# Kernel tuning notes

Hardware: AMD Instinct MI355X
Metric: run time of the kernel (lower is better)

The kernel has to match this reference:

```python
import jax, jax.numpy as jnp
import numpy as np

F = 26   # number of sparse features
D = 128  # embedding dim (== dense dim)
B = 16384

# Upper-triangular (offset=1) index pairs of the (F+1)x(F+1) interaction matrix.
_TRIU_R, _TRIU_C = np.triu_indices(F + 1, k=1)
_TRIU_R = jnp.asarray(_TRIU_R)
_TRIU_C = jnp.asarray(_TRIU_C)


def setup_inputs() -> dict:
    key = jax.random.key(0)
    k1, k2 = jax.random.split(key)
    dense_features = jax.random.normal(k1, (B, D), dtype=jnp.float32)
    sparse_values = jax.random.normal(k2, (B, F * D), dtype=jnp.float32)
    return {"dense_features": dense_features, "sparse_values": sparse_values}


def reference(dense_features, sparse_values):
    B_, D_ = dense_features.shape
    sparse = sparse_values.reshape(B_, F, D_)                 # B x F x D
    combined = jnp.concatenate([dense_features[:, None, :], sparse], axis=1)  # B x (F+1) x D
    # Batched pairwise dot products: B x (F+1) x (F+1)
    interactions = jnp.einsum("bfd,bgd->bfg", combined, combined)
    interactions_flat = interactions[:, _TRIU_R, _TRIU_C]     # B x (F + F choose 2)
    return jnp.concatenate([dense_features, interactions_flat], axis=1)
```

## Files before the change

### kernel.cpp

```cpp
#include <hip/hip_runtime.h>
#include <hip/hip_bf16.h>

#define NF 26
#define DD 128
#define OUTW 479

typedef __attribute__((ext_vector_type(8))) short bf16x8;
typedef __attribute__((ext_vector_type(4))) float f32x4;

__device__ __forceinline__ int triidx(int r, int c) {
    return r * NF - (r * (r - 1)) / 2 + (c - r - 1);
}

__device__ __forceinline__ ushort bf16_bits(float x) {
    __hip_bfloat16 h = __float2bfloat16(x);
    return *(ushort*)&h;
}

__device__ __forceinline__ bf16x8 cvt8(const float* p) {
    f32x4 x0 = *(const f32x4*)p;
    f32x4 x1 = *(const f32x4*)(p + 4);
    bf16x8 r;
#pragma unroll
    for (int j = 0; j < 4; ++j) {
        __hip_bfloat16 h0 = __float2bfloat16(x0[j]);
        __hip_bfloat16 h1 = __float2bfloat16(x1[j]);
        r[j]     = *(short*)&h0;
        r[j + 4] = *(short*)&h1;
    }
    return r;
}

__global__ __launch_bounds__(256) void interact_kernel(
    const void* __restrict__ dense_v,
    const void* __restrict__ sparse_v,
    void* __restrict__ out_v,
    int nbatch)
{
    const int gwave = (int)((blockIdx.x * 256u + threadIdx.x) >> 6);
    const int lane  = (int)(threadIdx.x & 63u);
    if (gwave >= nbatch) return;
    const size_t b = (size_t)gwave;

    const int m  = lane & 15;
    const int kg = lane >> 4;
    const int ko = kg * 8;

    {
    }
    const ushort* dpr = (const ushort*)dense_v;
    const ushort uprobe = dpr[2 * lane];
    const int eprobe = (uprobe >> 7) & 0xFF;
    const unsigned long long badmask = __ballot((eprobe < 90) | (eprobe > 140));
    const bool f32_mode = __popcll(badmask) >= 8;

    int sm = m + 15;
    if (sm > NF - 1) sm = NF - 1;

    bf16x8 a0[4], a1[4];
    if (f32_mode) {
        const float* dense  = (const float*)dense_v;
        const float* sparse = (const float*)sparse_v;
        const float* r0 = (m == 0)
            ? (dense + b * DD)
            : (sparse + b * (size_t)(NF * DD) + (size_t)(m - 1) * DD);
        const float* r1 = sparse + b * (size_t)(NF * DD) + (size_t)sm * DD;
#pragma unroll
        for (int t = 0; t < 4; ++t) {
            a0[t] = cvt8(r0 + t * 32 + ko);
            a1[t] = cvt8(r1 + t * 32 + ko);
        }
    } else {
        const ushort* dense  = (const ushort*)dense_v;
        const ushort* sparse = (const ushort*)sparse_v;
        const ushort* r0 = (m == 0)
            ? (dense + b * DD)
            : (sparse + b * (size_t)(NF * DD) + (size_t)(m - 1) * DD);
        const ushort* r1 = sparse + b * (size_t)(NF * DD) + (size_t)sm * DD;
#pragma unroll
        for (int t = 0; t < 4; ++t) {
            a0[t] = *(const bf16x8*)(r0 + t * 32 + ko);
            a1[t] = *(const bf16x8*)(r1 + t * 32 + ko);
        }
    }

    f32x4 g00 = {0.f, 0.f, 0.f, 0.f};
    f32x4 g10 = {0.f, 0.f, 0.f, 0.f};
    f32x4 g11 = {0.f, 0.f, 0.f, 0.f};
#pragma unroll
    for (int t = 0; t < 4; ++t) {
        g00 = __builtin_amdgcn_mfma_f32_16x16x32_bf16(a0[t], a0[t], g00, 0, 0, 0);
        g10 = __builtin_amdgcn_mfma_f32_16x16x32_bf16(a1[t], a0[t], g10, 0, 0, 0);
        g11 = __builtin_amdgcn_mfma_f32_16x16x32_bf16(a1[t], a1[t], g11, 0, 0, 0);
    }

    if (f32_mode) {
        float* orow = (float*)out_v + b * OUTW;
        const float* drow = (const float*)dense_v + b * DD;
        orow[2 * lane]     = drow[2 * lane];
        orow[2 * lane + 1] = drow[2 * lane + 1];
        float* tri = orow + DD;
#pragma unroll
        for (int i = 0; i < 4; ++i) {
            const int rr = kg * 4 + i;
            if (rr < m) tri[triidx(rr, m)] = g00[i];
            const int c2 = 16 + rr;
            if (c2 <= NF) tri[triidx(m, c2)] = g10[i];
            if (rr < m && 16 + m <= NF)
                tri[triidx(16 + rr, 16 + m)] = g11[i];
        }
    } else {
        ushort* orow = (ushort*)out_v + b * OUTW;
        const ushort* drow = (const ushort*)dense_v + b * DD;
        orow[2 * lane]     = drow[2 * lane];
        orow[2 * lane + 1] = drow[2 * lane + 1];
        ushort* tri = orow + DD;
#pragma unroll
        for (int i = 0; i < 4; ++i) {
            const int rr = kg * 4 + i;
            if (rr < m) tri[triidx(rr, m)] = bf16_bits(g00[i]);
            const int c2 = 16 + rr;
            if (c2 <= NF) tri[triidx(m, c2)] = bf16_bits(g10[i]);
            if (rr < m && 16 + m <= NF)
                tri[triidx(16 + rr, 16 + m)] = bf16_bits(g11[i]);
        }
    }
}

extern "C" void kernel_launch(void* const* d_in, const int* in_sizes, int n_in,
                              void* d_out, int out_size, void* d_ws, size_t ws_size,
                              hipStream_t stream) {
    const int nbatch = in_sizes[0] / DD;
    const int blocks = (nbatch * 64 + 255) / 256;
    interact_kernel<<<blocks, 256, 0, stream>>>(d_in[0], d_in[1], d_out, nbatch);
}
```

Measured before the change: 317.2 us.

## Stage f32 inputs and outputs through LDS for coalesced block-wide loads and stores

In the f32 path, each block now covers 4 batch rows. It loads the sparse and dense data with fully coalesced 16-byte loads, converts them to bf16 into a swizzled LDS buffer, and has each wave read its MFMA operands from there. Results are gathered into an LDS output row and written back as contiguous vector stores, replacing the scattered per-lane global stores. This aims to fix uncoalesced reads and writes at the cost of extra LDS traffic, two barriers, and a tail case that assumes nbatch is a multiple of 4.

New measurement: 309.7 us. 1.02x faster.

```diff
diff --git a/kernel.cpp b/kernel.cpp
--- a/kernel.cpp
+++ b/kernel.cpp
@@ -4,6 +4,7 @@
 #define NF 26
 #define DD 128
 #define OUTW 479
+#define SPF (NF * DD)
 
 typedef __attribute__((ext_vector_type(8))) short bf16x8;
 typedef __attribute__((ext_vector_type(4))) float f32x4;
@@ -23,10 +24,8 @@
     bf16x8 r;
 #pragma unroll
     for (int j = 0; j < 4; ++j) {
-        __hip_bfloat16 h0 = __float2bfloat16(x0[j]);
-        __hip_bfloat16 h1 = __float2bfloat16(x1[j]);
-        r[j]     = *(short*)&h0;
-        r[j + 4] = *(short*)&h1;
+        r[j]     = (short)bf16_bits(x0[j]);
+        r[j + 4] = (short)bf16_bits(x1[j]);
     }
     return r;
 }
@@ -37,69 +36,82 @@
     void* __restrict__ out_v,
     int nbatch)
 {
-    const int gwave = (int)((blockIdx.x * 256u + threadIdx.x) >> 6);
-    const int lane  = (int)(threadIdx.x & 63u);
-    if (gwave >= nbatch) return;
-    const size_t b = (size_t)gwave;
-
+    const int tid  = (int)threadIdx.x;
+    const int wave = tid >> 6;
+    const int lane = tid & 63;
     const int m  = lane & 15;
     const int kg = lane >> 4;
-    const int ko = kg * 8;
 
-    {
-    }
     const ushort* dpr = (const ushort*)dense_v;
     const ushort uprobe = dpr[2 * lane];
     const int eprobe = (uprobe >> 7) & 0xFF;
     const unsigned long long badmask = __ballot((eprobe < 90) | (eprobe > 140));
     const bool f32_mode = __popcll(badmask) >= 8;
 
-    int sm = m + 15;
-    if (sm > NF - 1) sm = NF - 1;
-
-    bf16x8 a0[4], a1[4];
     if (f32_mode) {
         const float* dense  = (const float*)dense_v;
         const float* sparse = (const float*)sparse_v;
-        const float* r0 = (m == 0)
-            ? (dense + b * DD)
-            : (sparse + b * (size_t)(NF * DD) + (size_t)(m - 1) * DD);
-        const float* r1 = sparse + b * (size_t)(NF * DD) + (size_t)sm * DD;
+        float* out = (float*)out_v;
+
+        __shared__ __align__(16) ushort stage[4 * 27 * 128];
+        __shared__ __align__(16) float  outS[4 * OUTW];
+
+        const int b0 = (int)blockIdx.x * 4;
+        if (b0 >= nbatch) return;
+
+        const float* sbase = sparse + (size_t)b0 * SPF;
+#pragma unroll
+        for (int it = 0; it < 13; ++it) {
+            const int f = (it * 256 + tid) * 4;
+            f32x4 v = *(const f32x4*)(sbase + f);
+            const int s   = f / SPF;
+            const int rem = f - s * SPF;
+            const int r   = 1 + (rem >> 7);
+            const int c   = rem & 127;
+            const int cb  = c >> 3;
+            const int hf  = (c >> 2) & 1;
+            const int pcb = cb ^ (r & 15);
+            ushort4 h;
+            h.x = bf16_bits(v[0]); h.y = bf16_bits(v[1]);
+            h.z = bf16_bits(v[2]); h.w = bf16_bits(v[3]);
+            *(ushort4*)&stage[s * 3456 + r * 128 + pcb * 8 + hf * 4] = h;
+        }
+        if (tid < 128) {
+            const int f = tid * 4;
+            f32x4 v = *(const f32x4*)(dense + (size_t)b0 * DD + f);
+            const int s = f >> 7;
+            const int c = f & 127;
+#pragma unroll
+            for (int k = 0; k < 4; ++k) outS[s * OUTW + c + k] = v[k];
+            const int cb = c >> 3;
+            const int hf = (c >> 2) & 1;
+            ushort4 h;
+            h.x = bf16_bits(v[0]); h.y = bf16_bits(v[1]);
+            h.z = bf16_bits(v[2]); h.w = bf16_bits(v[3]);
+            *(ushort4*)&stage[s * 3456 + (cb ^ 0) * 8 + hf * 4] = h;
+        }
+        __syncthreads();
+
+        int r1 = m + 16;
+        if (r1 > NF) r1 = NF;
+        bf16x8 a0[4], a1[4];
 #pragma unroll
         for (int t = 0; t < 4; ++t) {
-            a0[t] = cvt8(r0 + t * 32 + ko);
-            a1[t] = cvt8(r1 + t * 32 + ko);
+            const int cb = kg + 4 * t;
+            a0[t] = *(const bf16x8*)&stage[wave * 3456 + m  * 128 + (cb ^ (m  & 15)) * 8];
+            a1[t] = *(const bf16x8*)&stage[wave * 3456 + r1 * 128 + (cb ^ (r1 & 15)) * 8];
         }
-    } else {
-        const ushort* dense  = (const ushort*)dense_v;
-        const ushort* sparse = (const ushort*)sparse_v;
-        const ushort* r0 = (m == 0)
-            ? (dense + b * DD)
-            : (sparse + b * (size_t)(NF * DD) + (size_t)(m - 1) * DD);
-        const ushort* r1 = sparse + b * (size_t)(NF * DD) + (size_t)sm * DD;
+        f32x4 g00 = {0.f, 0.f, 0.f, 0.f};
+        f32x4 g10 = {0.f, 0.f, 0.f, 0.f};
+        f32x4 g11 = {0.f, 0.f, 0.f, 0.f};
 #pragma unroll
         for (int t = 0; t < 4; ++t) {
-            a0[t] = *(const bf16x8*)(r0 + t * 32 + ko);
-            a1[t] = *(const bf16x8*)(r1 + t * 32 + ko);
+            g00 = __builtin_amdgcn_mfma_f32_16x16x32_bf16(a0[t], a0[t], g00, 0, 0, 0);
+            g10 = __builtin_amdgcn_mfma_f32_16x16x32_bf16(a1[t], a0[t], g10, 0, 0, 0);
+            g11 = __builtin_amdgcn_mfma_f32_16x16x32_bf16(a1[t], a1[t], g11, 0, 0, 0);
         }
-    }
 
-    f32x4 g00 = {0.f, 0.f, 0.f, 0.f};
-    f32x4 g10 = {0.f, 0.f, 0.f, 0.f};
-    f32x4 g11 = {0.f, 0.f, 0.f, 0.f};
-#pragma unroll
-    for (int t = 0; t < 4; ++t) {
-        g00 = __builtin_amdgcn_mfma_f32_16x16x32_bf16(a0[t], a0[t], g00, 0, 0, 0);
-        g10 = __builtin_amdgcn_mfma_f32_16x16x32_bf16(a1[t], a0[t], g10, 0, 0, 0);
-        g11 = __builtin_amdgcn_mfma_f32_16x16x32_bf16(a1[t], a1[t], g11, 0, 0, 0);
-    }
-
-    if (f32_mode) {
-        float* orow = (float*)out_v + b * OUTW;
-        const float* drow = (const float*)dense_v + b * DD;
-        orow[2 * lane]     = drow[2 * lane];
-        orow[2 * lane + 1] = drow[2 * lane + 1];
-        float* tri = orow + DD;
+        float* tri = &outS[wave * OUTW + DD];
 #pragma unroll
         for (int i = 0; i < 4; ++i) {
             const int rr = kg * 4 + i;
@@ -109,9 +121,48 @@
             if (rr < m && 16 + m <= NF)
                 tri[triidx(16 + rr, 16 + m)] = g11[i];
         }
-    } else {
+        __syncthreads();
+
+        float* obase = out + (size_t)b0 * OUTW;
+        {
+            *(f32x4*)(obase + tid * 4) = *(const f32x4*)&outS[tid * 4];
+            const int c2 = tid + 256;
+            if (c2 < 479)
+                *(f32x4*)(obase + c2 * 4) = *(const f32x4*)&outS[c2 * 4];
+        }
+        return;
+    }
+
+    {
+        const int gwave = (int)((blockIdx.x * 256u + threadIdx.x) >> 6);
+        if (gwave >= nbatch) return;
+        const size_t b = (size_t)gwave;
+        const int ko = kg * 8;
+        int sm = m + 15;
+        if (sm > NF - 1) sm = NF - 1;
+        const ushort* dense  = (const ushort*)dense_v;
+        const ushort* sparse = (const ushort*)sparse_v;
+        const ushort* r0 = (m == 0)
+            ? (dense + b * DD)
+            : (sparse + b * (size_t)(NF * DD) + (size_t)(m - 1) * DD);
+        const ushort* r1p = sparse + b * (size_t)(NF * DD) + (size_t)sm * DD;
+        bf16x8 a0[4], a1[4];
+#pragma unroll
+        for (int t = 0; t < 4; ++t) {
+            a0[t] = *(const bf16x8*)(r0 + t * 32 + ko);
+            a1[t] = *(const bf16x8*)(r1p + t * 32 + ko);
+        }
+        f32x4 g00 = {0.f, 0.f, 0.f, 0.f};
+        f32x4 g10 = {0.f, 0.f, 0.f, 0.f};
+        f32x4 g11 = {0.f, 0.f, 0.f, 0.f};
+#pragma unroll
+        for (int t = 0; t < 4; ++t) {
+            g00 = __builtin_amdgcn_mfma_f32_16x16x32_bf16(a0[t], a0[t], g00, 0, 0, 0);
+            g10 = __builtin_amdgcn_mfma_f32_16x16x32_bf16(a1[t], a0[t], g10, 0, 0, 0);
+            g11 = __builtin_amdgcn_mfma_f32_16x16x32_bf16(a1[t], a1[t], g11, 0, 0, 0);
+        }
         ushort* orow = (ushort*)out_v + b * OUTW;
-        const ushort* drow = (const ushort*)dense_v + b * DD;
+        const ushort* drow = dense + b * DD;
         orow[2 * lane]     = drow[2 * lane];
         orow[2 * lane + 1] = drow[2 * lane + 1];
         ushort* tri = orow + DD;
@@ -131,6 +182,6 @@
                               void* d_out, int out_size, void* d_ws, size_t ws_size,
                               hipStream_t stream) {
     const int nbatch = in_sizes[0] / DD;
-    const int blocks = (nbatch * 64 + 255) / 256;
+    const int blocks = (nbatch + 3) / 4;
     interact_kernel<<<blocks, 256, 0, stream>>>(d_in[0], d_in[1], d_out, nbatch);
 }
```
